# Kernel optimization log

Hardware: AMD Instinct MI355X
Metric: run time of the kernel (lower is better)

The kernel has to match this reference:

```python
import jax, jax.numpy as jnp
import numpy as np

EPS = 1e-6


def setup_inputs() -> dict:
    key = jax.random.key(0)
    k1, k2 = jax.random.split(key)
    B, L, H = 256, 2048, 64
    h = jax.random.normal(k1, (B, L, H), dtype=jnp.float32)
    W = jax.random.normal(k2, (H, H), dtype=jnp.float32) * (1.0 / np.sqrt(H))
    b = jnp.zeros((H,), dtype=jnp.float32)
    return {"h": h, "W": W, "b": b}


def reference(h, W, b):
    # h: [B, L, H]; sequential delta-rule fast-weight memory with Hopfield gate.
    B, L, H = h.shape

    def step(M, k):
        # k == v == h[:, t, :]  (module uses the same vector for key and value)
        v_pred = jnp.einsum('bij,bj->bi', M, k)                    # M @ k
        denom = jnp.sum(k * k, axis=-1, keepdims=True) + EPS       # ||k||^2 + eps
        dM = jnp.einsum('bi,bj->bij', k - v_pred / denom, k)       # outer(v - v_pred/denom, k)
        M_new = M + dM
        # hopfield_energy(M) = -0.5 * ||M||^2; accept dM iff energy decreases,
        # i.e. iff ||M + dM||^2 > ||M||^2.
        gate = (jnp.sum(M_new * M_new, axis=(-2, -1)) >
                jnp.sum(M * M, axis=(-2, -1))).astype(M.dtype)[:, None, None]
        return M + gate * dM, None

    M0 = jnp.zeros((B, H, H), dtype=h.dtype)
    keys = jnp.swapaxes(h, 0, 1)[: L - 1]   # [L-1, B, H], time-major
    M, _ = jax.lax.scan(step, M0, keys)

    read = jnp.einsum('bij,bj->bi', M, h[:, -1, :])   # M @ h_last
    return read @ W.T + b                              # read_proj
```

## Files before the change

kernel.cpp:

```cpp
#include <hip/hip_runtime.h>

typedef float v4f __attribute__((ext_vector_type(4)));
typedef float v2f __attribute__((ext_vector_type(2)));
static constexpr float EPS = 1e-6f;

#define DPP_ADD(x, ctrl, rmask)                                               \
  x += __builtin_bit_cast(float, __builtin_amdgcn_update_dpp(                 \
           0, __builtin_bit_cast(int, x), ctrl, rmask, 0xf, true))

#define LVL10(ctrl, rmask, a, b, c, d, e, f, g, h, i, j)                      \
  DPP_ADD(a, ctrl, rmask); DPP_ADD(b, ctrl, rmask); DPP_ADD(c, ctrl, rmask);  \
  DPP_ADD(d, ctrl, rmask); DPP_ADD(e, ctrl, rmask); DPP_ADD(f, ctrl, rmask);  \
  DPP_ADD(g, ctrl, rmask); DPP_ADD(h, ctrl, rmask); DPP_ADD(i, ctrl, rmask);  \
  DPP_ADD(j, ctrl, rmask)

#define WAVE_RED10(a, b, c, d, e, f, g, h, i, j)                              \
  do {                                                                        \
    LVL10(0x111, 0xf, a, b, c, d, e, f, g, h, i, j);                          \
    LVL10(0x112, 0xf, a, b, c, d, e, f, g, h, i, j);                          \
    LVL10(0x114, 0xf, a, b, c, d, e, f, g, h, i, j);                          \
    LVL10(0x118, 0xf, a, b, c, d, e, f, g, h, i, j);                          \
    LVL10(0x142, 0xa, a, b, c, d, e, f, g, h, i, j);                          \
    LVL10(0x143, 0xc, a, b, c, d, e, f, g, h, i, j);                          \
  } while (0)

#define WAVE_RED3(a, b, c)                                                    \
  do {                                                                        \
    DPP_ADD(a, 0x111, 0xf); DPP_ADD(b, 0x111, 0xf); DPP_ADD(c, 0x111, 0xf);  \
    DPP_ADD(a, 0x112, 0xf); DPP_ADD(b, 0x112, 0xf); DPP_ADD(c, 0x112, 0xf);  \
    DPP_ADD(a, 0x114, 0xf); DPP_ADD(b, 0x114, 0xf); DPP_ADD(c, 0x114, 0xf);  \
    DPP_ADD(a, 0x118, 0xf); DPP_ADD(b, 0x118, 0xf); DPP_ADD(c, 0x118, 0xf);  \
    DPP_ADD(a, 0x142, 0xa); DPP_ADD(b, 0x142, 0xa); DPP_ADD(c, 0x142, 0xa);  \
    DPP_ADD(a, 0x143, 0xc); DPP_ADD(b, 0x143, 0xc); DPP_ADD(c, 0x143, 0xc);  \
  } while (0)

#define WAVE_RED2(a, b)                                                       \
  do {                                                                        \
    DPP_ADD(a, 0x111, 0xf); DPP_ADD(b, 0x111, 0xf);                           \
    DPP_ADD(a, 0x112, 0xf); DPP_ADD(b, 0x112, 0xf);                           \
    DPP_ADD(a, 0x114, 0xf); DPP_ADD(b, 0x114, 0xf);                           \
    DPP_ADD(a, 0x118, 0xf); DPP_ADD(b, 0x118, 0xf);                           \
    DPP_ADD(a, 0x142, 0xa); DPP_ADD(b, 0x142, 0xa);                           \
    DPP_ADD(a, 0x143, 0xc); DPP_ADD(b, 0x143, 0xc);                           \
  } while (0)

#define WAVE_RED1(a)                                                          \
  do {                                                                        \
    DPP_ADD(a, 0x111, 0xf); DPP_ADD(a, 0x112, 0xf); DPP_ADD(a, 0x114, 0xf);  \
    DPP_ADD(a, 0x118, 0xf); DPP_ADD(a, 0x142, 0xa); DPP_ADD(a, 0x143, 0xc);  \
  } while (0)

__device__ __forceinline__ float rl63(float x) {
  return __builtin_bit_cast(
      float, __builtin_amdgcn_readlane(__builtin_bit_cast(int, x), 63));
}

#define GLL(idx, slot)                                                        \
  __builtin_amdgcn_global_load_lds(                                           \
      (const __attribute__((address_space(1))) void*)(hb + (size_t)(idx) * 64 + lane), \
      (__attribute__((address_space(3))) void*)&kring[(slot)][0], 4, 0, 0)

#define DSR(dst, a, offb)                                                     \
  asm volatile("ds_read_b128 %0, %1 offset:%2"                                \
               : "=&v"(dst) : "v"(a), "i"(offb))
#define DSRB128(dst, a, offb)                                                 \
  asm volatile("ds_read_b128 %0, %1 offset:%2"                                \
               : "=&v"(dst) : "v"(a), "i"(offb))
#define DSRB64(dst, a, offb)                                                  \
  asm volatile("ds_read_b64 %0, %1 offset:%2"                                 \
               : "=&v"(dst) : "v"(a), "i"(offb))
#define DSW64(a, d, offb)                                                     \
  asm volatile("ds_write_b64 %0, %1 offset:%2"                                \
               :: "v"(a), "v"(d), "i"(offb) : "memory")
#define DSW32(a, d, offb)                                                     \
  asm volatile("ds_write_b32 %0, %1 offset:%2"                                \
               :: "v"(a), "v"(d), "i"(offb) : "memory")

#define DSR4(B, slot)                                                         \
  do {                                                                        \
    unsigned _a = kb + (unsigned)(slot) * 256u + woff;                        \
    DSR(B[0], _a, 0); DSR(B[1], _a, 16); DSR(B[2], _a, 32); DSR(B[3], _a, 48);\
  } while (0)
#define DSR1(dst, slot)                                                       \
  do {                                                                        \
    unsigned _a1 = kb + (unsigned)(slot) * 256u + laneb;                      \
    asm volatile("ds_read_b32 %0, %1" : "=&v"(dst) : "v"(_a1));               \
  } while (0)

#define SB __builtin_amdgcn_sched_barrier(0)
#define WAIT_LGKM(n)                                                          \
  do { asm volatile("s_waitcnt lgkmcnt(" #n ")" ::: "memory"); SB; } while (0)
#define WAIT_VM(n)                                                            \
  do { asm volatile("s_waitcnt vmcnt(" #n ")" ::: "memory"); SB; } while (0)
#define KEEP4(BK)                                                             \
  asm volatile("" :: "v"(BK[0]), "v"(BK[1]), "v"(BK[2]), "v"(BK[3]))

#define PAIR(UA, UB, NA, NB, PAR)                                             \
  do {                                                                        \
    float vp0 = A;                                      \
    float vp1 = fmaf(C_cur, u, A);                      \
    float u0 = fmaf(-r_nxt, vp0, e1);                                         \
    float u1 = fmaf(-r_nxt, vp1, e1);                                         \
    WAIT_LGKM(6);                                              \
    float D1own, D2own;                                                       \
    {                                                                         \
      v4f x0 = __builtin_elementwise_fma(m4[0], NA[0], v4f{0.f,0.f,0.f,0.f}); \
      v4f x1 = __builtin_elementwise_fma(m4[1], NA[1], v4f{0.f,0.f,0.f,0.f}); \
      x0 = __builtin_elementwise_fma(m4[2], NA[2], x0);                       \
      x1 = __builtin_elementwise_fma(m4[3], NA[3], x1);                       \
      v4f xs = x0 + x1;                                                       \
      D1own = (xs.x + xs.y) + (xs.z + xs.w);                                  \
    }                                                                         \
    WAIT_LGKM(2);                                              \
    {                                                                         \
      v4f y0 = __builtin_elementwise_fma(m4[0], NB[0], v4f{0.f,0.f,0.f,0.f}); \
      v4f y1 = __builtin_elementwise_fma(m4[1], NB[1], v4f{0.f,0.f,0.f,0.f}); \
      y0 = __builtin_elementwise_fma(m4[2], NB[2], y0);                       \
      y1 = __builtin_elementwise_fma(m4[3], NB[3], y1);                       \
      v4f ys = y0 + y1;                                                       \
      D2own = (ys.x + ys.y) + (ys.z + ys.w);                                  \
    }                                                                         \
    DSW64(pdx_w, ((v2f){D1own, D2own}), (PAR) * 2048);                        \
    if (w == 0) {                      \
      float wz = u  * fmaf(s2_cur, u,  2.0f * vp);                            \
      float z0 = u0 * fmaf(s2_nxt, u0, 2.0f * vp0);                           \
      float z1 = u1 * fmaf(s2_nxt, u1, 2.0f * vp1);                           \
      WAVE_RED3(wz, z0, z1);                                                  \
      if (lane == 63) {                                                       \
        DSW64(sc_a, ((v2f){wz, z0}), (PAR) * 48 + 0);                         \
        DSW32(sc_a, z1, (PAR) * 48 + 8);                                      \
      }                                                                       \
    } else if (w == 1) {                     \
      float pa = e2 * e2, pb = e3 * e3, pc = e2 * e3;                         \
      WAVE_RED3(pa, pb, pc);                                                  \
      if (lane == 63) {                                                       \
        DSW32(sc_a, pa, (PAR) * 48 + 12);                                     \
        DSW64(sc_a, ((v2f){pb, pc}), (PAR) * 48 + 16);                        \
      }                                                                       \
    } else if (w == 2) {                                       \
      float pa = e2 * e4, pb = e3 * e4;                                       \
      WAVE_RED2(pa, pb);                                                      \
      if (lane == 63) DSW64(sc_a, ((v2f){pa, pb}), (PAR) * 48 + 24);          \
    } else {                                                  \
      float pa = e2 * e5, pb = e3 * e5;                                       \
      WAVE_RED2(pa, pb);                                                      \
      if (lane == 63) DSW64(sc_a, ((v2f){pa, pb}), (PAR) * 48 + 32);          \
    }                                                                         \
    asm volatile("s_waitcnt lgkmcnt(0)" ::: "memory");    \
    __builtin_amdgcn_s_barrier();                                             \
    SB;                                                                       \
    v4f S0, S1; v2f S2, P0, P1, P2;                                           \
    DSRB128(S0, sc_a, (PAR) * 48 + 0);                                        \
    DSRB128(S1, sc_a, (PAR) * 48 + 16);                                       \
    DSRB64(S2, sc_a, (PAR) * 48 + 32);                                        \
    DSRB64(P0, pdx_r0, (PAR) * 2048);                                         \
    DSRB64(P1, pdx_r1, (PAR) * 2048);                                         \
    DSRB64(P2, pdx_r2, (PAR) * 2048);                                         \
    WAIT_LGKM(3);                                         \
    float zt = S0.x, z0s = S0.y, z1s = S0.z, s2a = S0.w;                      \
    float s2b = S1.x, C2s = S1.y, X02n = S1.z, C3s = S1.w;                    \
    bool gt = zt > 0.f;                                                       \
    float zsel = gt ? z1s : z0s;                                              \
    bool gt1 = zsel > 0.f;                                                    \
    float ga = gt ? u : 0.f;                                   \
    float usel = gt ? u1 : u0;                                                \
    float gb = gt1 ? usel : 0.f;                       \
    float r2 = 1.0f / (s2a + EPS);                                            \
    WAIT_LGKM(0);                                        \
    float X03n = S2.x, X13n = S2.y;                                           \
    float D1 = (D1own + P0.x) + (P1.x + P2.x);                                \
    float D2 = (D2own + P0.y) + (P1.y + P2.y);                                \
    float vp_n = fmaf(C_nxt, gb, fmaf(X02, ga, D1));            \
    float A_n  = fmaf(X13,  gb, fmaf(X03, ga, D2));      \
    float u_n  = fmaf(-r2, vp_n, e2);                            \
    {                                                                         \
      v4f gav = {ga, ga, ga, ga};                                             \
      m4[0] = __builtin_elementwise_fma(gav, UA[0], m4[0]);                   \
      m4[1] = __builtin_elementwise_fma(gav, UA[1], m4[1]);                   \
      m4[2] = __builtin_elementwise_fma(gav, UA[2], m4[2]);                   \
      m4[3] = __builtin_elementwise_fma(gav, UA[3], m4[3]);                   \
      v4f gbv = {gb, gb, gb, gb};                                             \
      m4[0] = __builtin_elementwise_fma(gbv, UB[0], m4[0]);                   \
      m4[1] = __builtin_elementwise_fma(gbv, UB[1], m4[1]);                   \
      m4[2] = __builtin_elementwise_fma(gbv, UB[2], m4[2]);                   \
      m4[3] = __builtin_elementwise_fma(gbv, UB[3], m4[3]);                   \
    }                                                                         \
    WAIT_VM(6);                                 \
    DSR4(UA, (t + 4) & 31);                    \
    DSR4(UB, (t + 5) & 31);                                                   \
    e1 = e3; e2 = e4; e3 = e5; e4 = eFp; e5 = eGp;     \
    DSR1(eFp, (t + 8) & 31);                                                  \
    DSR1(eGp, (t + 9) & 31);                                                  \
    {                                                                         \
      int i0 = t + 16; if (i0 > LM1) i0 = LM1;                                \
      int i1 = t + 17; if (i1 > LM1) i1 = LM1;                                \
      GLL(i0, (t + 16) & 31);                                                 \
      GLL(i1, (t + 17) & 31);                                                 \
    }                                                                         \
    SB;                                                                       \
    vp = vp_n; u = u_n; A = A_n;                                              \
    s2_cur = s2a; s2_nxt = s2b; r_nxt = 1.0f / (s2b + EPS);                   \
    C_cur = C2s; C_nxt = C3s; X02 = X02n; X03 = X03n; X13 = X13n;             \
    t += 2;                                                                   \
  } while (0)

__global__ __launch_bounds__(256, 1)
void delta_mem_seq(const float* __restrict__ h,
                   const float* __restrict__ W,
                   const float* __restrict__ bias,
                   float* __restrict__ out,
                   int L) {
  const int tid = threadIdx.x;
  const int w = tid >> 6;
  const int lane = tid & 63;
  __shared__ alignas(16) float kring[32][64];
  __shared__ alignas(16) v2f pdx[2][4][64];
  __shared__ alignas(16) float scal[2][12];
  __shared__ alignas(16) float rbuf[64];
  const float* __restrict__ hb = h + (size_t)blockIdx.x * (size_t)L * 64;
  const int LM1 = L - 1;

  const unsigned kb = (unsigned)(unsigned long long)
      (__attribute__((address_space(3))) const float*)&kring[0][0];
  const unsigned woff = (unsigned)(w << 6);
  const unsigned laneb = (unsigned)(lane << 2);
  const unsigned pb = (unsigned)(unsigned long long)
      (__attribute__((address_space(3))) const v2f*)&pdx[0][0][0];
  const unsigned pdx_w  = pb + (unsigned)(w << 9) + (unsigned)(lane << 3);
  const unsigned pdx_r0 = pb + (unsigned)(((w + 1) & 3) << 9) + (unsigned)(lane << 3);
  const unsigned pdx_r1 = pb + (unsigned)(((w + 2) & 3) << 9) + (unsigned)(lane << 3);
  const unsigned pdx_r2 = pb + (unsigned)(((w + 3) & 3) << 9) + (unsigned)(lane << 3);
  const unsigned sc_a = (unsigned)(unsigned long long)
      (__attribute__((address_space(3))) const float*)&scal[0][0];

  v4f m4[4];
#pragma unroll
  for (int q = 0; q < 4; ++q) m4[q] = v4f{0.f, 0.f, 0.f, 0.f};

#pragma unroll
  for (int i = 0; i < 16; ++i) {
    int idx = (i <= LM1) ? i : LM1;
    GLL(idx, i);
  }
  WAIT_VM(0);

  float e0 = kring[0][lane];
  float e1 = kring[1][lane], e2 = kring[2][lane], e3 = kring[3][lane];
  float e4 = kring[4][lane], e5 = kring[5][lane];

  float c0 = e0 * e0, c1 = e1 * e1, c2 = e0 * e1, c3 = e1 * e2;
  float c4 = e0 * e2, c5 = e0 * e3, c6 = e1 * e3;
  float c7 = 0.f, c8 = 0.f, c9 = 0.f;
  WAVE_RED10(c0, c1, c2, c3, c4, c5, c6, c7, c8, c9);
  float s2_cur = rl63(c0), s2_nxt = rl63(c1);
  float C_cur = rl63(c2), C_nxt = rl63(c3);
  float X02 = rl63(c4), X03 = rl63(c5), X13 = rl63(c6);
  float r_nxt = 1.0f / (s2_nxt + EPS);
  float vp = 0.f;
  float u = e0;
  float A = 0.f;
  int t = 0;

  v4f U0[4], U1[4], N0[4], N1[4];
  float eFp, eGp;
  SB;
  DSR4(U0, 0);
  DSR4(U1, 1);
  WAIT_LGKM(0);
  DSR4(N0, 2);
  DSR4(N1, 3);
  DSR1(eFp, 6);
  DSR1(eGp, 7);
  SB;

  while (t + 3 < LM1) {
    PAIR(U0, U1, N0, N1, 0);
    PAIR(N0, N1, U0, U1, 1);
  }
  if (t + 1 < LM1) PAIR(U0, U1, N0, N1, 0);

  asm volatile("s_waitcnt vmcnt(0) lgkmcnt(0)" ::: "memory");
  SB;
  KEEP4(U0); KEEP4(U1); KEEP4(N0); KEEP4(N1);
  asm volatile("" :: "v"(eFp), "v"(eGp));

  if (t < LM1) {
    float wz = u * fmaf(s2_cur, u, 2.0f * vp);
    WAVE_RED1(wz);
    float zt = rl63(wz);
    float coef = (zt > 0.f) ? C_cur : 0.f;
    vp = fmaf(coef, u, A);
  }

  if (w == 0) rbuf[lane] = vp;
  __syncthreads();

  if (w == 0) {
    const v4f* wv = (const v4f*)(W + lane * 64);
    const v4f* rv = (const v4f*)rbuf;
    v4f acc = v4f{0.f, 0.f, 0.f, 0.f};
#pragma unroll
    for (int q = 0; q < 16; ++q)
      acc = __builtin_elementwise_fma(wv[q], rv[q], acc);
    out[(size_t)blockIdx.x * 64 + lane] =
        bias[lane] + ((acc.x + acc.y) + (acc.z + acc.w));
  }
}

extern "C" void kernel_launch(void* const* d_in, const int* in_sizes, int n_in,
                              void* d_out, int out_size, void* d_ws, size_t ws_size,
                              hipStream_t stream) {
  const float* h    = (const float*)d_in[0];
  const float* W    = (const float*)d_in[1];
  const float* bias = (const float*)d_in[2];
  float* out = (float*)d_out;

  const int H = in_sizes[2];
  const int B = out_size / H;
  const int L = in_sizes[0] / (B * H);

  delta_mem_seq<<<B, 256, 0, stream>>>(h, W, bias, out, L);
}
```

Measured before the change: 718.5 us.

## Reduce gate scalars redundantly in every wave and move prefetch ahead of barrier wait

Each wave now computes the three gate reductions (wz, z0, z1) itself and reads them with readlane, so they no longer pass through shared memory. The next-step Gram scalars are spread across the four waves, which publish them to a compacted scalar buffer. The ring-buffer reads and global prefetch are issued right after the barrier, before the partial-product reads are consumed, and the scalar bookkeeping is done afterward. The aim is to shorten the critical path of the per-step barrier exchange, at the cost of redundant DPP reductions in every wave.

New measurement: 887.7 us. +23.6%, slower.

```diff
diff --git a/kernel.cpp b/kernel.cpp
--- a/kernel.cpp
+++ b/kernel.cpp
@@ -13,7 +13,6 @@
   DPP_ADD(d, ctrl, rmask); DPP_ADD(e, ctrl, rmask); DPP_ADD(f, ctrl, rmask);  \
   DPP_ADD(g, ctrl, rmask); DPP_ADD(h, ctrl, rmask); DPP_ADD(i, ctrl, rmask);  \
   DPP_ADD(j, ctrl, rmask)
-
 #define WAVE_RED10(a, b, c, d, e, f, g, h, i, j)                              \
   do {                                                                        \
     LVL10(0x111, 0xf, a, b, c, d, e, f, g, h, i, j);                          \
@@ -23,27 +22,24 @@
     LVL10(0x142, 0xa, a, b, c, d, e, f, g, h, i, j);                          \
     LVL10(0x143, 0xc, a, b, c, d, e, f, g, h, i, j);                          \
   } while (0)
-
-#define WAVE_RED3(a, b, c)                                                    \
-  do {                                                                        \
-    DPP_ADD(a, 0x111, 0xf); DPP_ADD(b, 0x111, 0xf); DPP_ADD(c, 0x111, 0xf);  \
-    DPP_ADD(a, 0x112, 0xf); DPP_ADD(b, 0x112, 0xf); DPP_ADD(c, 0x112, 0xf);  \
-    DPP_ADD(a, 0x114, 0xf); DPP_ADD(b, 0x114, 0xf); DPP_ADD(c, 0x114, 0xf);  \
-    DPP_ADD(a, 0x118, 0xf); DPP_ADD(b, 0x118, 0xf); DPP_ADD(c, 0x118, 0xf);  \
-    DPP_ADD(a, 0x142, 0xa); DPP_ADD(b, 0x142, 0xa); DPP_ADD(c, 0x142, 0xa);  \
-    DPP_ADD(a, 0x143, 0xc); DPP_ADD(b, 0x143, 0xc); DPP_ADD(c, 0x143, 0xc);  \
-  } while (0)
-
-#define WAVE_RED2(a, b)                                                       \
-  do {                                                                        \
-    DPP_ADD(a, 0x111, 0xf); DPP_ADD(b, 0x111, 0xf);                           \
-    DPP_ADD(a, 0x112, 0xf); DPP_ADD(b, 0x112, 0xf);                           \
-    DPP_ADD(a, 0x114, 0xf); DPP_ADD(b, 0x114, 0xf);                           \
-    DPP_ADD(a, 0x118, 0xf); DPP_ADD(b, 0x118, 0xf);                           \
-    DPP_ADD(a, 0x142, 0xa); DPP_ADD(b, 0x142, 0xa);                           \
-    DPP_ADD(a, 0x143, 0xc); DPP_ADD(b, 0x143, 0xc);                           \
-  } while (0)
-
+#define LVL5(ctrl, rmask, a, b, c, d, e)                                      \
+  DPP_ADD(a, ctrl, rmask); DPP_ADD(b, ctrl, rmask); DPP_ADD(c, ctrl, rmask);  \
+  DPP_ADD(d, ctrl, rmask); DPP_ADD(e, ctrl, rmask)
+#define WAVE_RED5(a, b, c, d, e)                                              \
+  do {                                                                        \
+    LVL5(0x111, 0xf, a, b, c, d, e); LVL5(0x112, 0xf, a, b, c, d, e);         \
+    LVL5(0x114, 0xf, a, b, c, d, e); LVL5(0x118, 0xf, a, b, c, d, e);         \
+    LVL5(0x142, 0xa, a, b, c, d, e); LVL5(0x143, 0xc, a, b, c, d, e);         \
+  } while (0)
+#define LVL4(ctrl, rmask, a, b, c, d)                                         \
+  DPP_ADD(a, ctrl, rmask); DPP_ADD(b, ctrl, rmask); DPP_ADD(c, ctrl, rmask);  \
+  DPP_ADD(d, ctrl, rmask)
+#define WAVE_RED4(a, b, c, d)                                                 \
+  do {                                                                        \
+    LVL4(0x111, 0xf, a, b, c, d); LVL4(0x112, 0xf, a, b, c, d);               \
+    LVL4(0x114, 0xf, a, b, c, d); LVL4(0x118, 0xf, a, b, c, d);               \
+    LVL4(0x142, 0xa, a, b, c, d); LVL4(0x143, 0xc, a, b, c, d);               \
+  } while (0)
 #define WAVE_RED1(a)                                                          \
   do {                                                                        \
     DPP_ADD(a, 0x111, 0xf); DPP_ADD(a, 0x112, 0xf); DPP_ADD(a, 0x114, 0xf);  \
@@ -61,9 +57,6 @@
       (__attribute__((address_space(3))) void*)&kring[(slot)][0], 4, 0, 0)
 
 #define DSR(dst, a, offb)                                                     \
-  asm volatile("ds_read_b128 %0, %1 offset:%2"                                \
-               : "=&v"(dst) : "v"(a), "i"(offb))
-#define DSRB128(dst, a, offb)                                                 \
   asm volatile("ds_read_b128 %0, %1 offset:%2"                                \
                : "=&v"(dst) : "v"(a), "i"(offb))
 #define DSRB64(dst, a, offb)                                                  \
@@ -101,6 +94,11 @@
     float vp1 = fmaf(C_cur, u, A);                      \
     float u0 = fmaf(-r_nxt, vp0, e1);                                         \
     float u1 = fmaf(-r_nxt, vp1, e1);                                         \
+    float wz = u  * fmaf(s2_cur, u,  2.0f * vp);                              \
+    float z0 = u0 * fmaf(s2_nxt, u0, 2.0f * vp0);                             \
+    float z1 = u1 * fmaf(s2_nxt, u1, 2.0f * vp1);                             \
+    float pS2a = e2 * e2, pS2b = e3 * e3, pC2 = e2 * e3, pX02 = e2 * e4;      \
+    float pC3 = e3 * e4, pX03 = e2 * e5, pX13 = e3 * e5;                      \
     WAIT_LGKM(6);                                              \
     float D1own, D2own;                                                       \
     {                                                                         \
@@ -111,7 +109,7 @@
       v4f xs = x0 + x1;                                                       \
       D1own = (xs.x + xs.y) + (xs.z + xs.w);                                  \
     }                                                                         \
-    WAIT_LGKM(2);                                              \
+    WAIT_LGKM(2);                              \
     {                                                                         \
       v4f y0 = __builtin_elementwise_fma(m4[0], NB[0], v4f{0.f,0.f,0.f,0.f}); \
       v4f y1 = __builtin_elementwise_fma(m4[1], NB[1], v4f{0.f,0.f,0.f,0.f}); \
@@ -121,58 +119,26 @@
       D2own = (ys.x + ys.y) + (ys.z + ys.w);                                  \
     }                                                                         \
     DSW64(pdx_w, ((v2f){D1own, D2own}), (PAR) * 2048);                        \
-    if (w == 0) {                      \
-      float wz = u  * fmaf(s2_cur, u,  2.0f * vp);                            \
-      float z0 = u0 * fmaf(s2_nxt, u0, 2.0f * vp0);                           \
-      float z1 = u1 * fmaf(s2_nxt, u1, 2.0f * vp1);                           \
-      WAVE_RED3(wz, z0, z1);                                                  \
-      if (lane == 63) {                                                       \
-        DSW64(sc_a, ((v2f){wz, z0}), (PAR) * 48 + 0);                         \
-        DSW32(sc_a, z1, (PAR) * 48 + 8);                                      \
-      }                                                                       \
-    } else if (w == 1) {                     \
-      float pa = e2 * e2, pb = e3 * e3, pc = e2 * e3;                         \
-      WAVE_RED3(pa, pb, pc);                                                  \
-      if (lane == 63) {                                                       \
-        DSW32(sc_a, pa, (PAR) * 48 + 12);                                     \
-        DSW64(sc_a, ((v2f){pb, pc}), (PAR) * 48 + 16);                        \
-      }                                                                       \
-    } else if (w == 2) {                                       \
-      float pa = e2 * e4, pb = e3 * e4;                                       \
-      WAVE_RED2(pa, pb);                                                      \
-      if (lane == 63) DSW64(sc_a, ((v2f){pa, pb}), (PAR) * 48 + 24);          \
-    } else {                                                  \
-      float pa = e2 * e5, pb = e3 * e5;                                       \
-      WAVE_RED2(pa, pb);                                                      \
-      if (lane == 63) DSW64(sc_a, ((v2f){pa, pb}), (PAR) * 48 + 32);          \
-    }                                                                         \
-    asm volatile("s_waitcnt lgkmcnt(0)" ::: "memory");    \
-    __builtin_amdgcn_s_barrier();                                             \
-    SB;                                                                       \
-    v4f S0, S1; v2f S2, P0, P1, P2;                                           \
-    DSRB128(S0, sc_a, (PAR) * 48 + 0);                                        \
-    DSRB128(S1, sc_a, (PAR) * 48 + 16);                                       \
-    DSRB64(S2, sc_a, (PAR) * 48 + 32);                                        \
-    DSRB64(P0, pdx_r0, (PAR) * 2048);                                         \
-    DSRB64(P1, pdx_r1, (PAR) * 2048);                                         \
-    DSRB64(P2, pdx_r2, (PAR) * 2048);                                         \
-    WAIT_LGKM(3);                                         \
-    float zt = S0.x, z0s = S0.y, z1s = S0.z, s2a = S0.w;                      \
-    float s2b = S1.x, C2s = S1.y, X02n = S1.z, C3s = S1.w;                    \
+                         \
+    if (w == 0)      { WAVE_RED5(wz, z0, z1, pS2a, pS2b); }                   \
+    else if (w == 1) { WAVE_RED5(wz, z0, z1, pC2, pX02); }                    \
+    else if (w == 2) { WAVE_RED5(wz, z0, z1, pC3, pX03); }                    \
+    else             { WAVE_RED4(wz, z0, z1, pX13); }                         \
+    if (lane == 63) {                                                         \
+      if (w == 0)      DSW64(sc_pub, ((v2f){pS2a, pS2b}), (PAR) * 32);        \
+      else if (w == 1) DSW64(sc_pub, ((v2f){pC2, pX02}), (PAR) * 32);         \
+      else if (w == 2) DSW64(sc_pub, ((v2f){pC3, pX03}), (PAR) * 32);         \
+      else             DSW32(sc_pub, pX13, (PAR) * 32);                       \
+    }                                                                         \
+                          \
+    float zt = rl63(wz);                                                      \
+    float z0s = rl63(z0), z1s = rl63(z1);                                     \
     bool gt = zt > 0.f;                                                       \
     float zsel = gt ? z1s : z0s;                                              \
     bool gt1 = zsel > 0.f;                                                    \
     float ga = gt ? u : 0.f;                                   \
     float usel = gt ? u1 : u0;                                                \
     float gb = gt1 ? usel : 0.f;                       \
-    float r2 = 1.0f / (s2a + EPS);                                            \
-    WAIT_LGKM(0);                                        \
-    float X03n = S2.x, X13n = S2.y;                                           \
-    float D1 = (D1own + P0.x) + (P1.x + P2.x);                                \
-    float D2 = (D2own + P0.y) + (P1.y + P2.y);                                \
-    float vp_n = fmaf(C_nxt, gb, fmaf(X02, ga, D1));            \
-    float A_n  = fmaf(X13,  gb, fmaf(X03, ga, D2));      \
-    float u_n  = fmaf(-r2, vp_n, e2);                            \
     {                                                                         \
       v4f gav = {ga, ga, ga, ga};                                             \
       m4[0] = __builtin_elementwise_fma(gav, UA[0], m4[0]);                   \
@@ -185,22 +151,38 @@
       m4[2] = __builtin_elementwise_fma(gbv, UB[2], m4[2]);                   \
       m4[3] = __builtin_elementwise_fma(gbv, UB[3], m4[3]);                   \
     }                                                                         \
-    WAIT_VM(6);                                 \
-    DSR4(UA, (t + 4) & 31);                    \
-    DSR4(UB, (t + 5) & 31);                                                   \
-    e1 = e3; e2 = e4; e3 = e5; e4 = eFp; e5 = eGp;     \
+    WAIT_LGKM(0);                              \
+    __builtin_amdgcn_s_barrier();                                             \
+    SB;                                                                       \
+    v4f S0, S1; v2f P0, P1, P2;                                               \
+    DSR(S0, sc_a, (PAR) * 32 + 0);                                            \
+    DSR(S1, sc_a, (PAR) * 32 + 16);                                           \
+    DSRB64(P0, pdx_r0, (PAR) * 2048);                                         \
+    DSRB64(P1, pdx_r1, (PAR) * 2048);                                         \
+    DSRB64(P2, pdx_r2, (PAR) * 2048);                              \
+    WAIT_VM(6);                    \
+    DSR4(UA, (t + 4) & 31);      \
+    DSR4(UB, (t + 5) & 31);                                       \
+    float e2c = e2;                                                           \
+    e1 = e3; e2 = e4; e3 = e5; e4 = eFp; e5 = eGp;                            \
     DSR1(eFp, (t + 8) & 31);                                                  \
-    DSR1(eGp, (t + 9) & 31);                                                  \
+    DSR1(eGp, (t + 9) & 31);                                      \
     {                                                                         \
       int i0 = t + 16; if (i0 > LM1) i0 = LM1;                                \
       int i1 = t + 17; if (i1 > LM1) i1 = LM1;                                \
       GLL(i0, (t + 16) & 31);                                                 \
       GLL(i1, (t + 17) & 31);                                                 \
     }                                                                         \
-    SB;                                                                       \
+    WAIT_LGKM(10);         \
+    float D1 = (D1own + P0.x) + (P1.x + P2.x);                                \
+    float D2 = (D2own + P0.y) + (P1.y + P2.y);                                \
+    float vp_n = fmaf(C_nxt, gb, fmaf(X02, ga, D1));            \
+    float A_n  = fmaf(X13,  gb, fmaf(X03, ga, D2));      \
+    float u_n  = fmaf(-(1.0f / (S0.x + EPS)), vp_n, e2c);        \
+    s2_cur = S0.x; s2_nxt = S0.y; r_nxt = 1.0f / (S0.y + EPS);                \
+    C_cur = S0.z; C_nxt = S1.x;                                               \
+    X02 = S0.w; X03 = S1.y; X13 = S1.z;                                       \
     vp = vp_n; u = u_n; A = A_n;                                              \
-    s2_cur = s2a; s2_nxt = s2b; r_nxt = 1.0f / (s2b + EPS);                   \
-    C_cur = C2s; C_nxt = C3s; X02 = X02n; X03 = X03n; X13 = X13n;             \
     t += 2;                                                                   \
   } while (0)
 
@@ -215,7 +197,7 @@
   const int lane = tid & 63;
   __shared__ alignas(16) float kring[32][64];
   __shared__ alignas(16) v2f pdx[2][4][64];
-  __shared__ alignas(16) float scal[2][12];
+  __shared__ alignas(16) float scal[2][8];
   __shared__ alignas(16) float rbuf[64];
   const float* __restrict__ hb = h + (size_t)blockIdx.x * (size_t)L * 64;
   const int LM1 = L - 1;
@@ -232,6 +214,7 @@
   const unsigned pdx_r2 = pb + (unsigned)(((w + 3) & 3) << 9) + (unsigned)(lane << 3);
   const unsigned sc_a = (unsigned)(unsigned long long)
       (__attribute__((address_space(3))) const float*)&scal[0][0];
+  const unsigned sc_pub = sc_a + (unsigned)(w << 3);
 
   v4f m4[4];
 #pragma unroll
@@ -244,9 +227,9 @@
   }
   WAIT_VM(0);
 
+  float e1 = kring[1][lane], e2 = kring[2][lane];
+  float e3 = kring[3][lane], e4 = kring[4][lane], e5 = kring[5][lane];
   float e0 = kring[0][lane];
-  float e1 = kring[1][lane], e2 = kring[2][lane], e3 = kring[3][lane];
-  float e4 = kring[4][lane], e5 = kring[5][lane];
 
   float c0 = e0 * e0, c1 = e1 * e1, c2 = e0 * e1, c3 = e1 * e2;
   float c4 = e0 * e2, c5 = e0 * e3, c6 = e1 * e3;
@@ -264,13 +247,10 @@
   v4f U0[4], U1[4], N0[4], N1[4];
   float eFp, eGp;
   SB;
-  DSR4(U0, 0);
-  DSR4(U1, 1);
+  DSR4(U0, 0); DSR4(U1, 1);
   WAIT_LGKM(0);
-  DSR4(N0, 2);
-  DSR4(N1, 3);
-  DSR1(eFp, 6);
-  DSR1(eGp, 7);
+  DSR4(N0, 2); DSR4(N1, 3);
+  DSR1(eFp, 6); DSR1(eGp, 7);
   SB;
 
   while (t + 3 < LM1) {
```
